# Performance work log

Hardware: AMD Instinct MI355X
Metric: run time of the kernel (lower is better)

## Reference

```python
import jax, jax.numpy as jnp
import numpy as np

DIM = 512
NUM_HEADS = 8
HEAD_DIM = DIM // NUM_HEADS
SCALE = HEAD_DIM ** -0.5
B, N = 8, 1024


def setup_inputs() -> dict:
    key = jax.random.key(0)
    k1, k2, k3, k4, k5 = jax.random.split(key, 5)
    x = jax.random.normal(k1, (B, N, DIM), dtype=jnp.float32)
    rpe_bias = jax.random.normal(k2, (1, NUM_HEADS, N, N), dtype=jnp.float32)
    # torch Linear weights: [out_features, in_features], y = x @ W.T
    qkv_w = jax.random.normal(k3, (3 * DIM, DIM), dtype=jnp.float32) * (DIM ** -0.5)
    proj_w = jax.random.normal(k4, (DIM, DIM), dtype=jnp.float32) * (DIM ** -0.5)
    proj_b = jax.random.normal(k5, (DIM,), dtype=jnp.float32) * 0.01
    return {"x": x, "rpe_bias": rpe_bias, "qkv_w": qkv_w, "proj_w": proj_w, "proj_b": proj_b}


def reference(x, rpe_bias, qkv_w, proj_w, proj_b):
    b, n, c = x.shape
    h, d = NUM_HEADS, HEAD_DIM
    # qkv projection (no bias): [B,N,3C] -> [3,B,H,N,D]
    qkv = (x @ qkv_w.T).reshape(b, n, 3, h, d).transpose(2, 0, 3, 1, 4)
    q, k, v = qkv[0], qkv[1], qkv[2]
    attn = jnp.einsum('bhnd,bhmd->bhnm', q, k) * SCALE + rpe_bias
    attn = jax.nn.softmax(attn, axis=-1)  # dropout p=0 -> identity
    out = jnp.einsum('bhnm,bhmd->bhnd', attn, v)
    out = out.transpose(0, 2, 1, 3).reshape(b, n, c)
    return out @ proj_w.T + proj_b
```

## Files before the change

kernel.cpp:

```cpp
#include <hip/hip_runtime.h>
#include <hip/hip_bf16.h>

#define B_    8
#define N_    1024
#define DIM_  512
#define H_    8
#define DH_   64
#define SCALE_ 0.125f

typedef unsigned short u16;
typedef __attribute__((ext_vector_type(8))) short bf16x8;
typedef __attribute__((ext_vector_type(4))) short bf16x4;
typedef __attribute__((ext_vector_type(4))) float f32x4;

__device__ __forceinline__ u16 f2bf(float f) {
  union { float f; unsigned u; } v; v.f = f;
  return (u16)((v.u + 0x7fffu + ((v.u >> 16) & 1u)) >> 16);
}
__device__ __forceinline__ unsigned pack2(float a, float b) {
  return (unsigned)f2bf(a) | ((unsigned)f2bf(b) << 16);
}
__device__ __forceinline__ void cp16(const void* g, void* l) {
  __builtin_amdgcn_global_load_lds(
      (const __attribute__((address_space(1))) unsigned*)g,
      (__attribute__((address_space(3))) unsigned*)l, 16, 0, 0);
}

__global__ __launch_bounds__(256) void convert_kernel(
    const float* __restrict__ X, const float* __restrict__ Wq,
    const float* __restrict__ Wp, u16* __restrict__ Xb,
    u16* __restrict__ Wqb, u16* __restrict__ Wpb) {
  const int NX4 = (B_ * N_ * DIM_) / 4;
  const int NQ4 = (3 * DIM_ * DIM_) / 4;
  const int NP4 = (DIM_ * DIM_) / 4;
  const int total = NX4 + NQ4 + NP4;
  const int stride = gridDim.x * 256;
  for (int i = blockIdx.x * 256 + threadIdx.x; i < total; i += stride) {
    const float* s; u16* d; int off;
    if (i < NX4)            { s = X;  d = Xb;  off = i; }
    else if (i < NX4 + NQ4) { s = Wq; d = Wqb; off = i - NX4; }
    else                    { s = Wp; d = Wpb; off = i - NX4 - NQ4; }
    float4 f = *(const float4*)(s + (size_t)off * 4);
    uint2 u; u.x = pack2(f.x, f.y); u.y = pack2(f.z, f.w);
    *(uint2*)(d + (size_t)off * 4) = u;
  }
}

__global__ __launch_bounds__(256, 4) void qkv_gemm(
    const u16* __restrict__ Ab, const u16* __restrict__ Bb,
    u16* __restrict__ Q, u16* __restrict__ K, u16* __restrict__ Vt) {
  __shared__ __align__(16) u16 sA[128 * 64];
  __shared__ __align__(16) u16 sB[64 * 64];
  const int t = threadIdx.x;
  const int wv = t >> 6, lane = t & 63, quad = (lane >> 4) & 3, l15 = lane & 15;
  const int m0 = blockIdx.y * 128;
  const int n0 = blockIdx.x * 64;

  const int srow = lane >> 3;
  const int schunk = (lane & 7) ^ srow;
  const size_t ga = (size_t)(m0 + srow) * DIM_ + schunk * 8;
  const size_t gb = (size_t)(n0 + srow) * DIM_ + schunk * 8;

  f32x4 zero = {0.f, 0.f, 0.f, 0.f};
  f32x4 acc[2][4];
#pragma unroll
  for (int i = 0; i < 2; i++)
#pragma unroll
    for (int j = 0; j < 4; j++) acc[i][j] = zero;

  for (int k0 = 0; k0 < DIM_; k0 += 64) {
    __syncthreads();
#pragma unroll
    for (int i = 0; i < 4; i++) {
      const int rb = 32 * wv + 8 * i;
      cp16(Ab + ga + (size_t)rb * DIM_ + k0, &sA[rb * 64]);
    }
#pragma unroll
    for (int i = 0; i < 2; i++) {
      const int rb = 16 * wv + 8 * i;
      cp16(Bb + gb + (size_t)rb * DIM_ + k0, &sB[rb * 64]);
    }
    __syncthreads();
#pragma unroll
    for (int ks = 0; ks < 2; ks++) {
      bf16x8 af[2], bfv[4];
#pragma unroll
      for (int i = 0; i < 2; i++)
        af[i] = *(const bf16x8*)&sA[(wv * 32 + 16 * i + l15) * 64 +
                                    (((ks << 2) | quad) ^ (l15 & 7)) * 8];
#pragma unroll
      for (int j = 0; j < 4; j++)
        bfv[j] = *(const bf16x8*)&sB[(16 * j + l15) * 64 +
                                     (((ks << 2) | quad) ^ (l15 & 7)) * 8];
#pragma unroll
      for (int i = 0; i < 2; i++)
#pragma unroll
        for (int j = 0; j < 4; j++)
          acc[i][j] = __builtin_amdgcn_mfma_f32_16x16x32_bf16(af[i], bfv[j], acc[i][j], 0, 0, 0);
    }
  }

  const int tsel = n0 >> 9;
#pragma unroll
  for (int j = 0; j < 4; j++) {
    const int jg = n0 + 16 * j + l15;
    const int h = (jg >> 6) & 7, d = jg & 63;
#pragma unroll
    for (int i = 0; i < 2; i++) {
      const int mbase = m0 + wv * 32 + 16 * i + quad * 4;
      const int b = mbase >> 10, nb = mbase & 1023;
      const size_t bh = (size_t)(b * H_ + h);
      if (tsel == 2) {
        ushort4 v4;
        v4.x = f2bf(acc[i][j][0]); v4.y = f2bf(acc[i][j][1]);
        v4.z = f2bf(acc[i][j][2]); v4.w = f2bf(acc[i][j][3]);
        *(ushort4*)&Vt[(bh * DH_ + d) * N_ + nb] = v4;
      } else {
        u16* dst = (tsel == 0 ? Q : K);
#pragma unroll
        for (int rr = 0; rr < 4; rr++)
          dst[(bh * N_ + nb + rr) * DH_ + d] = f2bf(acc[i][j][rr]);
      }
    }
  }
}

__global__ __launch_bounds__(256, 4) void attn_kernel(
    const u16* __restrict__ Q, const u16* __restrict__ K,
    const u16* __restrict__ Vt, const float* __restrict__ bias,
    u16* __restrict__ AO) {
  __shared__ __align__(16) u16 sK[64 * 64];
  __shared__ __align__(16) u16 sV[64 * 64];
  const int t = threadIdx.x;
  const int wv = t >> 6, lane = t & 63, quad = (lane >> 4) & 3, l15 = lane & 15;

  const int bid = blockIdx.x;
  const int h = bid & 7;
  const int s = bid >> 3;
  const int nx = s >> 3;
  const int b = s & 7;
  const int n0 = nx << 6;
  const int bh = b * H_ + h;
  const int r = t >> 2, c = (t & 3) << 4;

  const int qg = n0 + 16 * wv + l15;
  bf16x8 qf0, qf1;
  {
    const u16* qa = Q + (((size_t)bh << 10) + qg) * DH_ + (quad << 3);
    qf0 = *(const bf16x8*)qa; qf1 = *(const bf16x8*)(qa + 32);
  }

  const float* bp = bias + (((size_t)h << 10) + qg) * N_ + (quad << 2);
  const u16* kbase = K + (((size_t)bh << 10) + r) * DH_ + c;
  const u16* vbase = Vt + (((size_t)bh << 6) + r) * N_ + c;

  const int so0 = r * 128 + ((((t & 3) << 5)) ^ ((r & 7) << 4));
  const int so1 = r * 128 + ((((t & 3) << 5) + 16) ^ ((r & 7) << 4));
  const int rx = (l15 & 7) << 4;
  const int frow = l15 * 128;
  const int vhalf = (quad & 1) << 3;

  f32x4 zero = {0.f, 0.f, 0.f, 0.f};
  f32x4 O[4];
  O[0] = zero; O[1] = zero; O[2] = zero; O[3] = zero;
  float lsum = 0.f;

  uint4 k0r = *(const uint4*)kbase, k1r = *(const uint4*)(kbase + 8);
  uint4 v0r = *(const uint4*)vbase, v1r = *(const uint4*)(vbase + 8);

  for (int kt = 0; kt < 16; kt++) {
    __syncthreads();
    *(uint4*)((char*)sK + so0) = k0r; *(uint4*)((char*)sK + so1) = k1r;
    *(uint4*)((char*)sV + so0) = v0r; *(uint4*)((char*)sV + so1) = v1r;
    if (kt < 15) {
      const u16* kn = kbase + (size_t)(kt + 1) * 64 * DH_;
      const u16* vn = vbase + (kt + 1) * 64;
      k0r = *(const uint4*)kn; k1r = *(const uint4*)(kn + 8);
      v0r = *(const uint4*)vn; v1r = *(const uint4*)(vn + 8);
    }
    float4 b4[4];
#pragma unroll
    for (int cb = 0; cb < 4; cb++)
      b4[cb] = *(const float4*)(bp + (kt << 6) + 16 * cb);
    __syncthreads();

    bf16x8 kf[8];
#pragma unroll
    for (int ks = 0; ks < 2; ks++)
#pragma unroll
      for (int cb = 0; cb < 4; cb++)
        kf[ks * 4 + cb] = *(const bf16x8*)((const char*)sK + cb * 2048 + frow +
                                           (((ks << 6) | (quad << 4)) ^ rx));

    f32x4 S[4];
    S[0] = zero; S[1] = zero; S[2] = zero; S[3] = zero;
    __builtin_amdgcn_s_setprio(1);
#pragma unroll
    for (int ks = 0; ks < 2; ks++) {
      const bf16x8 qf = ks ? qf1 : qf0;
#pragma unroll
      for (int cb = 0; cb < 4; cb++)
        S[cb] = __builtin_amdgcn_mfma_f32_16x16x32_bf16(kf[ks * 4 + cb], qf, S[cb], 0, 0, 0);
    }
    __builtin_amdgcn_s_setprio(0);

    bf16x4 p[4];
#pragma unroll
    for (int cb = 0; cb < 4; cb++) {
      float p0 = __expf(fmaf(S[cb][0], SCALE_, b4[cb].x));
      float p1 = __expf(fmaf(S[cb][1], SCALE_, b4[cb].y));
      float p2 = __expf(fmaf(S[cb][2], SCALE_, b4[cb].z));
      float p3 = __expf(fmaf(S[cb][3], SCALE_, b4[cb].w));
      lsum += (p0 + p1) + (p2 + p3);
      uint2 pk; pk.x = pack2(p0, p1); pk.y = pack2(p2, p3);
      p[cb] = __builtin_bit_cast(bf16x4, pk);
    }

    __builtin_amdgcn_s_setprio(1);
#pragma unroll
    for (int cbp = 0; cbp < 4; cbp++) {
      bf16x4 vf[4];
#pragma unroll
      for (int cb = 0; cb < 4; cb++) {
        const int ch = ((((2 * cb + (quad >> 1)) << 4)) ^ rx) + vhalf;
        vf[cb] = *(const bf16x4*)((const char*)sV + cbp * 2048 + frow + ch);
      }
#pragma unroll
      for (int cb = 0; cb < 4; cb++)
        O[cbp] = __builtin_amdgcn_mfma_f32_16x16x16bf16_1k(vf[cb], p[cb], O[cbp], 0, 0, 0);
    }
    __builtin_amdgcn_s_setprio(0);
  }

  lsum += __shfl_xor(lsum, 16);
  lsum += __shfl_xor(lsum, 32);
  const float inv = 1.f / lsum;
#pragma unroll
  for (int cb = 0; cb < 4; cb++) {
    ushort4 o4;
    o4.x = f2bf(O[cb][0] * inv); o4.y = f2bf(O[cb][1] * inv);
    o4.z = f2bf(O[cb][2] * inv); o4.w = f2bf(O[cb][3] * inv);
    *(ushort4*)&AO[(((size_t)bh << 10 | (size_t)0) * 0) +
                   (((size_t)b << 10) + qg) * DIM_ + h * DH_ + 16 * cb + (quad << 2)] = o4;
  }
}

__global__ __launch_bounds__(256, 4) void proj_gemm(
    const u16* __restrict__ Ab, const u16* __restrict__ Bb,
    const float* __restrict__ Pb, float* __restrict__ Out) {
  __shared__ __align__(16) u16 sA[128 * 64];
  __shared__ __align__(16) u16 sB[64 * 64];
  const int t = threadIdx.x;
  const int wv = t >> 6, lane = t & 63, quad = (lane >> 4) & 3, l15 = lane & 15;
  const int m0 = blockIdx.y * 128;
  const int n0 = blockIdx.x * 64;

  const int srow = lane >> 3;
  const int schunk = (lane & 7) ^ srow;
  const size_t ga = (size_t)(m0 + srow) * DIM_ + schunk * 8;
  const size_t gb = (size_t)(n0 + srow) * DIM_ + schunk * 8;

  f32x4 zero = {0.f, 0.f, 0.f, 0.f};
  f32x4 acc[2][4];
#pragma unroll
  for (int i = 0; i < 2; i++)
#pragma unroll
    for (int j = 0; j < 4; j++) acc[i][j] = zero;

  for (int k0 = 0; k0 < DIM_; k0 += 64) {
    __syncthreads();
#pragma unroll
    for (int i = 0; i < 4; i++) {
      const int rb = 32 * wv + 8 * i;
      cp16(Ab + ga + (size_t)rb * DIM_ + k0, &sA[rb * 64]);
    }
#pragma unroll
    for (int i = 0; i < 2; i++) {
      const int rb = 16 * wv + 8 * i;
      cp16(Bb + gb + (size_t)rb * DIM_ + k0, &sB[rb * 64]);
    }
    __syncthreads();
#pragma unroll
    for (int ks = 0; ks < 2; ks++) {
      bf16x8 af[2], bfv[4];
#pragma unroll
      for (int i = 0; i < 2; i++)
        af[i] = *(const bf16x8*)&sA[(wv * 32 + 16 * i + l15) * 64 +
                                    (((ks << 2) | quad) ^ (l15 & 7)) * 8];
#pragma unroll
      for (int j = 0; j < 4; j++)
        bfv[j] = *(const bf16x8*)&sB[(16 * j + l15) * 64 +
                                     (((ks << 2) | quad) ^ (l15 & 7)) * 8];
#pragma unroll
      for (int i = 0; i < 2; i++)
#pragma unroll
        for (int j = 0; j < 4; j++)
          acc[i][j] = __builtin_amdgcn_mfma_f32_16x16x32_bf16(af[i], bfv[j], acc[i][j], 0, 0, 0);
    }
  }

#pragma unroll
  for (int j = 0; j < 4; j++) {
    const int jg = n0 + 16 * j + l15;
    const float pb = Pb[jg];
#pragma unroll
    for (int i = 0; i < 2; i++) {
      const int mbase = m0 + wv * 32 + 16 * i + quad * 4;
#pragma unroll
      for (int rr = 0; rr < 4; rr++)
        Out[(size_t)(mbase + rr) * DIM_ + jg] = acc[i][j][rr] + pb;
    }
  }
}

extern "C" void kernel_launch(void* const* d_in, const int* in_sizes, int n_in,
                              void* d_out, int out_size, void* d_ws, size_t ws_size,
                              hipStream_t stream) {
  const float* x      = (const float*)d_in[0];
  const float* rpe    = (const float*)d_in[1];
  const float* qkv_w  = (const float*)d_in[2];
  const float* proj_w = (const float*)d_in[3];
  const float* proj_b = (const float*)d_in[4];
  float* out = (float*)d_out;

  const size_t perbuf = (size_t)B_ * N_ * DIM_;
  u16* Xb  = (u16*)d_ws;
  u16* Q   = Xb + perbuf;
  u16* K   = Q + perbuf;
  u16* Vt  = K + perbuf;
  u16* Wqb = Vt + perbuf;
  u16* Wpb = Wqb + (size_t)3 * DIM_ * DIM_;
  u16* AO  = Xb;

  convert_kernel<<<2560, 256, 0, stream>>>(x, qkv_w, proj_w, Xb, Wqb, Wpb);
  qkv_gemm<<<dim3(24, 64), 256, 0, stream>>>(Xb, Wqb, Q, K, Vt);
  attn_kernel<<<1024, 256, 0, stream>>>(Q, K, Vt, rpe, AO);
  proj_gemm<<<dim3(8, 64), 256, 0, stream>>>(AO, Wpb, proj_b, out);
}
```

Before: 173.7 us.

## Double-buffer GEMM LDS tiles and widen attention blocks to 128 queries

Both GEMM kernels now keep two LDS tile buffers, issuing the next k-tile's async global-to-LDS copies before computing the current one, with manual s_waitcnt and s_barrier, and they raise MFMA priority with s_setprio. The attention kernel uses 512-thread blocks covering 128 query rows, so each staged K/V tile is shared by eight waves instead of four and every thread loads one 16-byte chunk per tile. This is meant to hide global load latency in the GEMMs and halve K/V reloads in attention, at the cost of more LDS per GEMM block (lower occupancy bound) and fewer, larger attention blocks.

```diff
diff --git a/kernel.cpp b/kernel.cpp
--- a/kernel.cpp
+++ b/kernel.cpp
@@ -46,11 +46,11 @@
   }
 }
 
-__global__ __launch_bounds__(256, 4) void qkv_gemm(
+__global__ __launch_bounds__(256, 3) void qkv_gemm(
     const u16* __restrict__ Ab, const u16* __restrict__ Bb,
     u16* __restrict__ Q, u16* __restrict__ K, u16* __restrict__ Vt) {
-  __shared__ __align__(16) u16 sA[128 * 64];
-  __shared__ __align__(16) u16 sB[64 * 64];
+  __shared__ __align__(16) u16 sA[2][128 * 64];
+  __shared__ __align__(16) u16 sB[2][64 * 64];
   const int t = threadIdx.x;
   const int wv = t >> 6, lane = t & 63, quad = (lane >> 4) & 3, l15 = lane & 15;
   const int m0 = blockIdx.y * 128;
@@ -68,43 +68,57 @@
 #pragma unroll
     for (int j = 0; j < 4; j++) acc[i][j] = zero;
 
-  for (int k0 = 0; k0 < DIM_; k0 += 64) {
-    __syncthreads();
+  auto stage = [&](int buf, int k0) {
 #pragma unroll
     for (int i = 0; i < 4; i++) {
       const int rb = 32 * wv + 8 * i;
-      cp16(Ab + ga + (size_t)rb * DIM_ + k0, &sA[rb * 64]);
+      cp16(Ab + ga + (size_t)rb * DIM_ + k0, &sA[buf][rb * 64]);
     }
 #pragma unroll
     for (int i = 0; i < 2; i++) {
       const int rb = 16 * wv + 8 * i;
-      cp16(Bb + gb + (size_t)rb * DIM_ + k0, &sB[rb * 64]);
-    }
-    __syncthreads();
+      cp16(Bb + gb + (size_t)rb * DIM_ + k0, &sB[buf][rb * 64]);
+    }
+  };
+
+  stage(0, 0);
+  for (int kt = 0; kt < 8; kt++) {
+    const int cur = kt & 1;
+    asm volatile("s_barrier" ::: "memory");
+    if (kt < 7) {
+      stage(cur ^ 1, (kt + 1) * 64);
+      asm volatile("s_waitcnt vmcnt(6)" ::: "memory");
+    } else {
+      asm volatile("s_waitcnt vmcnt(0)" ::: "memory");
+    }
+    asm volatile("s_barrier" ::: "memory");
 #pragma unroll
     for (int ks = 0; ks < 2; ks++) {
       bf16x8 af[2], bfv[4];
 #pragma unroll
       for (int i = 0; i < 2; i++)
-        af[i] = *(const bf16x8*)&sA[(wv * 32 + 16 * i + l15) * 64 +
-                                    (((ks << 2) | quad) ^ (l15 & 7)) * 8];
+        af[i] = *(const bf16x8*)&sA[cur][(wv * 32 + 16 * i + l15) * 64 +
+                                        (((ks << 2) | quad) ^ (l15 & 7)) * 8];
 #pragma unroll
       for (int j = 0; j < 4; j++)
-        bfv[j] = *(const bf16x8*)&sB[(16 * j + l15) * 64 +
-                                     (((ks << 2) | quad) ^ (l15 & 7)) * 8];
+        bfv[j] = *(const bf16x8*)&sB[cur][(16 * j + l15) * 64 +
+                                         (((ks << 2) | quad) ^ (l15 & 7)) * 8];
+      __builtin_amdgcn_s_setprio(1);
 #pragma unroll
       for (int i = 0; i < 2; i++)
 #pragma unroll
         for (int j = 0; j < 4; j++)
           acc[i][j] = __builtin_amdgcn_mfma_f32_16x16x32_bf16(af[i], bfv[j], acc[i][j], 0, 0, 0);
+      __builtin_amdgcn_s_setprio(0);
     }
   }
 
   const int tsel = n0 >> 9;
+  const int h = (n0 >> 6) & 7;
 #pragma unroll
   for (int j = 0; j < 4; j++) {
     const int jg = n0 + 16 * j + l15;
-    const int h = (jg >> 6) & 7, d = jg & 63;
+    const int d = jg & 63;
 #pragma unroll
     for (int i = 0; i < 2; i++) {
       const int mbase = m0 + wv * 32 + 16 * i + quad * 4;
@@ -125,23 +139,23 @@
   }
 }
 
-__global__ __launch_bounds__(256, 4) void attn_kernel(
+__global__ __launch_bounds__(512, 4) void attn_kernel(
     const u16* __restrict__ Q, const u16* __restrict__ K,
     const u16* __restrict__ Vt, const float* __restrict__ bias,
     u16* __restrict__ AO) {
   __shared__ __align__(16) u16 sK[64 * 64];
   __shared__ __align__(16) u16 sV[64 * 64];
   const int t = threadIdx.x;
-  const int wv = t >> 6, lane = t & 63, quad = (lane >> 4) & 3, l15 = lane & 15;
+  const int wv = t >> 6;
+  const int lane = t & 63, quad = (lane >> 4) & 3, l15 = lane & 15;
 
   const int bid = blockIdx.x;
   const int h = bid & 7;
   const int s = bid >> 3;
   const int nx = s >> 3;
   const int b = s & 7;
-  const int n0 = nx << 6;
+  const int n0 = nx << 7;
   const int bh = b * H_ + h;
-  const int r = t >> 2, c = (t & 3) << 4;
 
   const int qg = n0 + 16 * wv + l15;
   bf16x8 qf0, qf1;
@@ -151,11 +165,12 @@
   }
 
   const float* bp = bias + (((size_t)h << 10) + qg) * N_ + (quad << 2);
-  const u16* kbase = K + (((size_t)bh << 10) + r) * DH_ + c;
-  const u16* vbase = Vt + (((size_t)bh << 6) + r) * N_ + c;
-
-  const int so0 = r * 128 + ((((t & 3) << 5)) ^ ((r & 7) << 4));
-  const int so1 = r * 128 + ((((t & 3) << 5) + 16) ^ ((r & 7) << 4));
+
+  const int r = t >> 3, c8 = t & 7;
+  const u16* kbase = K + (((size_t)bh << 10) + r) * DH_ + (c8 << 3);
+  const u16* vbase = Vt + (((size_t)bh << 6) + r) * N_ + (c8 << 3);
+  const int so = r * 128 + ((c8 ^ (r & 7)) << 4);
+
   const int rx = (l15 & 7) << 4;
   const int frow = l15 * 128;
   const int vhalf = (quad & 1) << 3;
@@ -165,18 +180,16 @@
   O[0] = zero; O[1] = zero; O[2] = zero; O[3] = zero;
   float lsum = 0.f;
 
-  uint4 k0r = *(const uint4*)kbase, k1r = *(const uint4*)(kbase + 8);
-  uint4 v0r = *(const uint4*)vbase, v1r = *(const uint4*)(vbase + 8);
+  uint4 kr = *(const uint4*)kbase;
+  uint4 vr = *(const uint4*)vbase;
 
   for (int kt = 0; kt < 16; kt++) {
     __syncthreads();
-    *(uint4*)((char*)sK + so0) = k0r; *(uint4*)((char*)sK + so1) = k1r;
-    *(uint4*)((char*)sV + so0) = v0r; *(uint4*)((char*)sV + so1) = v1r;
+    *(uint4*)((char*)sK + so) = kr;
+    *(uint4*)((char*)sV + so) = vr;
     if (kt < 15) {
-      const u16* kn = kbase + (size_t)(kt + 1) * 64 * DH_;
-      const u16* vn = vbase + (kt + 1) * 64;
-      k0r = *(const uint4*)kn; k1r = *(const uint4*)(kn + 8);
-      v0r = *(const uint4*)vn; v1r = *(const uint4*)(vn + 8);
+      kr = *(const uint4*)(kbase + (size_t)(kt + 1) * 64 * DH_);
+      vr = *(const uint4*)(vbase + (kt + 1) * 64);
     }
     float4 b4[4];
 #pragma unroll
@@ -240,16 +253,15 @@
     ushort4 o4;
     o4.x = f2bf(O[cb][0] * inv); o4.y = f2bf(O[cb][1] * inv);
     o4.z = f2bf(O[cb][2] * inv); o4.w = f2bf(O[cb][3] * inv);
-    *(ushort4*)&AO[(((size_t)bh << 10 | (size_t)0) * 0) +
-                   (((size_t)b << 10) + qg) * DIM_ + h * DH_ + 16 * cb + (quad << 2)] = o4;
-  }
-}
-
-__global__ __launch_bounds__(256, 4) void proj_gemm(
+    *(ushort4*)&AO[(((size_t)b << 10) + qg) * DIM_ + h * DH_ + 16 * cb + (quad << 2)] = o4;
+  }
+}
+
+__global__ __launch_bounds__(256, 3) void proj_gemm(
     const u16* __restrict__ Ab, const u16* __restrict__ Bb,
     const float* __restrict__ Pb, float* __restrict__ Out) {
-  __shared__ __align__(16) u16 sA[128 * 64];
-  __shared__ __align__(16) u16 sB[64 * 64];
+  __shared__ __align__(16) u16 sA[2][128 * 64];
+  __shared__ __align__(16) u16 sB[2][64 * 64];
   const int t = threadIdx.x;
   const int wv = t >> 6, lane = t & 63, quad = (lane >> 4) & 3, l15 = lane & 15;
   const int m0 = blockIdx.y * 128;
@@ -267,35 +279,48 @@
 #pragma unroll
     for (int j = 0; j < 4; j++) acc[i][j] = zero;
 
-  for (int k0 = 0; k0 < DIM_; k0 += 64) {
-    __syncthreads();
+  auto stage = [&](int buf, int k0) {
 #pragma unroll
     for (int i = 0; i < 4; i++) {
       const int rb = 32 * wv + 8 * i;
-      cp16(Ab + ga + (size_t)rb * DIM_ + k0, &sA[rb * 64]);
+      cp16(Ab + ga + (size_t)rb * DIM_ + k0, &sA[buf][rb * 64]);
     }
 #pragma unroll
     for (int i = 0; i < 2; i++) {
       const int rb = 16 * wv + 8 * i;
-      cp16(Bb + gb + (size_t)rb * DIM_ + k0, &sB[rb * 64]);
-    }
-    __syncthreads();
+      cp16(Bb + gb + (size_t)rb * DIM_ + k0, &sB[buf][rb * 64]);
+    }
+  };
+
+  stage(0, 0);
+  for (int kt = 0; kt < 8; kt++) {
+    const int cur = kt & 1;
+    asm volatile("s_barrier" ::: "memory");
+    if (kt < 7) {
+      stage(cur ^ 1, (kt + 1) * 64);
+      asm volatile("s_waitcnt vmcnt(6)" ::: "memory");
+    } else {
+      asm volatile("s_waitcnt vmcnt(0)" ::: "memory");
+    }
+    asm volatile("s_barrier" ::: "memory");
 #pragma unroll
     for (int ks = 0; ks < 2; ks++) {
       bf16x8 af[2], bfv[4];
 #pragma unroll
       for (int i = 0; i < 2; i++)
-        af[i] = *(const bf16x8*)&sA[(wv * 32 + 16 * i + l15) * 64 +
-                                    (((ks << 2) | quad) ^ (l15 & 7)) * 8];
+        af[i] = *(const bf16x8*)&sA[cur][(wv * 32 + 16 * i + l15) * 64 +
+                                        (((ks << 2) | quad) ^ (l15 & 7)) * 8];
 #pragma unroll
       for (int j = 0; j < 4; j++)
-        bfv[j] = *(const bf16x8*)&sB[(16 * j + l15) * 64 +
-                                     (((ks << 2) | quad) ^ (l15 & 7)) * 8];
+        bfv[j] = *(const bf16x8*)&sB[cur][(16 * j + l15) * 64 +
+                                         (((ks << 2) | quad) ^ (l15 & 7)) * 8];
+      __builtin_amdgcn_s_setprio(1);
 #pragma unroll
       for (int i = 0; i < 2; i++)
 #pragma unroll
         for (int j = 0; j < 4; j++)
           acc[i][j] = __builtin_amdgcn_mfma_f32_16x16x32_bf16(af[i], bfv[j], acc[i][j], 0, 0, 0);
+      __builtin_amdgcn_s_setprio(0);
     }
   }
 
@@ -334,6 +359,6 @@
 
   convert_kernel<<<2560, 256, 0, stream>>>(x, qkv_w, proj_w, Xb, Wqb, Wpb);
   qkv_gemm<<<dim3(24, 64), 256, 0, stream>>>(Xb, Wqb, Q, K, Vt);
-  attn_kernel<<<1024, 256, 0, stream>>>(Q, K, Vt, rpe, AO);
+  attn_kernel<<<512, 512, 0, stream>>>(Q, K, Vt, rpe, AO);
   proj_gemm<<<dim3(8, 64), 256, 0, stream>>>(AO, Wpb, proj_b, out);
 }
```

Measured after the change: 167.0 us. -3.9%, faster.
